# Performance work log

Measured on AMD Instinct MI355X. Metric: run time of the kernel, lower is better.

Reference implementation:

```python
import jax, jax.numpy as jnp
import numpy as np

EPS = 1e-5
B, N, E, D, ED, F = 4096, 22, 42, 128, 32, 2048

def _ln(x, g, b):
    m = jnp.mean(x, axis=-1, keepdims=True)
    v = jnp.var(x, axis=-1, keepdims=True)
    return (x - m) * jax.lax.rsqrt(v + EPS) * g + b

def setup_inputs() -> dict:
    key = jax.random.key(0)
    ks = jax.random.split(key, 24)
    def rn(k, shp, scale=0.05):
        return jax.random.normal(k, shp, dtype=jnp.float32) * scale
    return {
        "node_features": jax.random.normal(ks[0], (B, N, D), dtype=jnp.float32),
        "edge_attr": jax.random.normal(ks[1], (B, E, ED), dtype=jnp.float32),
        "aggregation_matrix": jax.random.uniform(ks[2], (N, E), dtype=jnp.float32),
        "source_indices": jax.random.randint(ks[3], (E,), 0, N, dtype=jnp.int32),
        "target_indices": jax.random.randint(ks[4], (E,), 0, N, dtype=jnp.int32),
        # edge MLP: Linear(2D+ED -> 4*ED), ReLU, Linear(4*ED -> ED)
        "ew1": rn(ks[5], (2 * D + ED, 4 * ED)), "eb1": jnp.zeros((4 * ED,), jnp.float32),
        "ew2": rn(ks[6], (4 * ED, ED)), "eb2": jnp.zeros((ED,), jnp.float32),
        # message projection ED -> D
        "pw": rn(ks[7], (ED, D)), "pb": jnp.zeros((D,), jnp.float32),
        # gated update gates: 2D -> D each
        "rw": rn(ks[8], (2 * D, D)), "rb": jnp.zeros((D,), jnp.float32),
        "uw": rn(ks[9], (2 * D, D)), "ub": jnp.zeros((D,), jnp.float32),
        "cw": rn(ks[10], (2 * D, D)), "cb": jnp.zeros((D,), jnp.float32),
        # layernorms
        "g1": jnp.ones((D,), jnp.float32), "be1": jnp.zeros((D,), jnp.float32),
        "g2": jnp.ones((D,), jnp.float32), "be2": jnp.zeros((D,), jnp.float32),
        # FFN D -> F -> D
        "fw1": rn(ks[11], (D, F)), "fb1": jnp.zeros((F,), jnp.float32),
        "fw2": rn(ks[12], (F, D)), "fb2": jnp.zeros((D,), jnp.float32),
    }

def reference(node_features, edge_attr, aggregation_matrix, source_indices, target_indices,
              ew1, eb1, ew2, eb2, pw, pb, rw, rb, uw, ub, cw, cb,
              g1, be1, g2, be2, fw1, fb1, fw2, fb2):
    normed = _ln(node_features, g1, be1)                      # [B,N,D]
    src = jnp.take(normed, source_indices, axis=1)            # [B,E,D]
    tgt = jnp.take(normed, target_indices, axis=1)            # [B,E,D]
    combined = jnp.concatenate([src, tgt, edge_attr], axis=-1)  # [B,E,2D+ED]
    h = jax.nn.relu(combined @ ew1 + eb1)
    edge_messages = h @ ew2 + eb2                             # [B,E,ED]
    aggregated = jnp.einsum('ne,bed->bnd', aggregation_matrix, edge_messages)  # [B,N,ED]
    projected = aggregated @ pw + pb                          # [B,N,D]
    # GRU-style gated update
    nm = jnp.concatenate([normed, projected], axis=-1)
    reset = jax.nn.sigmoid(nm @ rw + rb)
    update = jax.nn.sigmoid(nm @ uw + ub)
    rc = jnp.concatenate([reset * normed, projected], axis=-1)
    cand = jnp.tanh(rc @ cw + cb)
    x = node_features + (1.0 - update) * normed + update * cand
    # norm + FFN (dropout = identity in eval mode)
    n2 = _ln(x, g2, be2)
    ff = jax.nn.gelu(n2 @ fw1 + fb1, approximate=False) @ fw2 + fb2
    return (x + ff, edge_messages)
```

## Files before the change

### kernel.cpp

```cpp
#include <hip/hip_runtime.h>
#include <math.h>

#define NB 4096
#define NN 22
#define NE 42
#define DD 128
#define ED2 32
#define HH 128
#define FF 2048
#define HCHUNKS 32

typedef float f32x4 __attribute__((ext_vector_type(4)));
typedef short s16x8 __attribute__((ext_vector_type(8)));

__device__ __forceinline__ float sigmoidf_(float x){ return 1.f/(1.f+__expf(-x)); }

__device__ __forceinline__ unsigned short f2bf(float f){
  unsigned u = __float_as_uint(f);
  u += 0x7fffu + ((u >> 16) & 1u);
  return (unsigned short)(u >> 16);
}
__device__ __forceinline__ float bf2f(unsigned short h){
  return __uint_as_float(((unsigned)h) << 16);
}
__device__ __forceinline__ float gelu_f(float x){
  float x2 = x*x;
  float inner = fmaf(0.044715f*x2, x, x);
  float p = __builtin_amdgcn_exp2f(2.3022085f*inner);
  float t = __builtin_amdgcn_rcpf(p + 1.f);
  return fmaf(-x, t, x);
}

__device__ __forceinline__ void gld16(const void* g, void* l){
  __builtin_amdgcn_global_load_lds((__attribute__((address_space(1))) void*)g,
                                   (__attribute__((address_space(3))) void*)l, 16, 0, 0);
}
template<int BYTES, int NW>
__device__ __forceinline__ void stage_lds(void* lbase, const void* gbase, int wave, int lane){
  const int per = BYTES / NW;
  const int ni  = per / 1024;
  const char* g = (const char*)gbase + wave*per + lane*16;
  char* l = (char*)lbase + wave*per;
  #pragma unroll
  for (int i=0;i<ni;i++) gld16(g + i*1024, l + i*1024);
}

#define S_VMCNT(N) { asm volatile("s_waitcnt vmcnt(" #N ")" ::: "memory"); __builtin_amdgcn_sched_barrier(0); }
#define S_LGKM0()  { asm volatile("s_waitcnt lgkmcnt(0)" ::: "memory"); __builtin_amdgcn_sched_barrier(0); }
#define RAW_BAR()  { asm volatile("s_waitcnt lgkmcnt(0)" ::: "memory"); __builtin_amdgcn_sched_barrier(0); __builtin_amdgcn_s_barrier(); __builtin_amdgcn_sched_barrier(0); }

__device__ __forceinline__ int fragidx128(int c, int k){
  return ((c>>4)*4 + (k>>5))*512 + (((k>>3)&3)*16 + (c&15))*8 + (k&7);
}
__device__ __forceinline__ int fragidx64(int c, int k){
  return ((c>>4)*2 + (k>>5))*512 + (((k>>3)&3)*16 + (c&15))*8 + (k&7);
}

__global__ __launch_bounds__(256) void wconv_kernel(
    const float* __restrict__ fw1, const float* __restrict__ fw2,
    const float* __restrict__ ew1, const float* __restrict__ ew2,
    const float* __restrict__ rw, const float* __restrict__ uw, const float* __restrict__ cw,
    const float* __restrict__ pw, const float* __restrict__ aggm,
    unsigned short* __restrict__ w1t, unsigned short* __restrict__ w2b,
    unsigned short* __restrict__ ewc, unsigned short* __restrict__ ew2c,
    unsigned short* __restrict__ gw,
    unsigned short* __restrict__ tailf, unsigned short* __restrict__ pwf,
    unsigned short* __restrict__ aggmf)
{
  const int idx = blockIdx.x*256 + threadIdx.x;
  {
    const int k = idx >> 11, j = idx & 2047;
    w1t[(j>>7)*16384 + fragidx128(j&127, k)] = f2bf(fw1[idx]);
  }
  {
    const int kg = idx >> 7, c = idx & 127;
    w2b[(kg>>6)*8192 + fragidx64(c, kg&63)] = f2bf(fw2[idx]);
  }
  if (idx < 32768) {
    const int c2 = idx >> 7, k = idx & 127;
    const int part = c2 >> 7, c = c2 & 127;
    const float v = ew1[(part*128 + k)*DD + c];
    ewc[part*16384 + ((k>>5)*8 + (c>>4))*512 + (((k>>3)&3)*16 + (c&15))*8 + (k&7)] = f2bf(v);
  }
  if (idx < 4096) {
    const int m = idx & 31, k = idx >> 5;
    ew2c[fragidx128(m, k)] = f2bf(ew2[k*ED2 + m]);
  }
  if (idx < 4096) {
    const int k = idx >> 7, c = idx & 127;
    const int u = (c>>4)*512 + ((k>>3)*16 + (c&15))*8 + (k&7);
    tailf[u] = f2bf(ew1[(256 + k)*DD + c]);
    pwf[u]  = f2bf(pw[k*DD + c]);
  }
  if (idx < 2048) {
    const int n = idx >> 6, e = idx & 63;
    const float v = (n < NN && e < NE) ? aggm[n*NE + e] : 0.f;
    aggmf[(n>>4)*1024 + (e>>5)*512 + (((e>>3)&3)*16 + (n&15))*8 + (e&7)] = f2bf(v);
  }
  if (idx < 98304) {
    const int gate = idx >> 15;
    const int rem  = idx & 32767;
    const int half = rem >> 14, c = (rem >> 7) & 127, k = rem & 127;
    const float* wsrc = (gate==0) ? rw : ((gate==1) ? uw : cw);
    const float v = wsrc[(half*128 + k)*128 + c];
    gw[gate*32768 + half*16384 + (k>>6)*8192 + fragidx64(c, k&63)] = f2bf(v);
  }
}

__global__ __launch_bounds__(512) void edge_mfma_kernel(
    const float* __restrict__ nf, const float* __restrict__ ea,
    const int* __restrict__ src, const int* __restrict__ tgt,
    const float* __restrict__ eb1, const float* __restrict__ eb2,
    const float* __restrict__ pb,
    const unsigned short* __restrict__ ewc2,
    const unsigned short* __restrict__ ew2c,
    const unsigned short* __restrict__ tailf,
    const unsigned short* __restrict__ pwf,
    const unsigned short* __restrict__ aggmf,
    const float* __restrict__ g1, const float* __restrict__ be1,
    float* __restrict__ out_em, float* __restrict__ out_x)
{
  const int t = threadIdx.x, lane = t & 63, wave = t >> 6;
  const int wv = wave & 3;
  const int bb = wave >> 2;
  const int b  = blockIdx.x*2 + bb;
  const int th = t & 255;

  __shared__ __align__(16) char s_lds[76160];
  unsigned short* s_w0  = (unsigned short*)(s_lds);
  unsigned short* s_w1  = (unsigned short*)(s_lds + 16384);
  unsigned short* s_emf = (unsigned short*)(s_lds + 16384 + bb*4096);
  unsigned short* s_ew2 = (unsigned short*)(s_lds + 32768);
  unsigned short* s_agm = (unsigned short*)(s_lds + 40960);
  char*           s_a   = s_lds + 45056 + bb*8192;
  char*           s_h   = s_lds + 45056 + bb*12288;
  unsigned short* s_eaf = (unsigned short*)(s_lds + 69632 + bb*3072);
  unsigned short* s_agf = s_eaf;
  int*            s_srcA= (int*)(s_lds + 75776);
  int*            s_tgtA= (int*)(s_lds + 75968);

  stage_lds<16384,8>(s_w0, ewc2, wave, lane);
  stage_lds<8192,8>(s_ew2, ew2c, wave, lane);
  if (wave < 4) stage_lds<4096,4>(s_agm, aggmf, wave, lane);

  for (int r = wv; r < NN; r += 4) {
    const float* row = nf + ((size_t)b*NN + r)*DD;
    float x0 = row[lane], x1 = row[lane+64];
    float s = x0+x1, ss = x0*x0+x1*x1;
    #pragma unroll
    for (int off=32; off>=1; off>>=1) { s += __shfl_xor(s,off); ss += __shfl_xor(ss,off); }
    float m = s*(1.f/128.f);
    float inv = rsqrtf(ss*(1.f/128.f)-m*m + 1e-5f);
    float n0 = (x0-m)*inv*g1[lane]+be1[lane];
    float n1 = (x1-m)*inv*g1[lane+64]+be1[lane+64];
    char* base = s_a + r*256;
    const int sw = (r&7)<<4;
    *(unsigned short*)(base + ((lane*2)      ^ sw)) = f2bf(n0);
    *(unsigned short*)(base + (((lane+64)*2) ^ sw)) = f2bf(n1);
  }
  for (int i=th; i<640; i+=256) ((float*)(s_a + NN*256))[i] = 0.f;

  if (t < 48) { s_srcA[t] = (t < NE) ? src[t] : NN; s_tgtA[t] = (t < NE) ? tgt[t] : NN; }

  if (th < 168) {
    const int e = th >> 2, kb = th & 3;
    const float* p = ea + ((size_t)b*NE + e)*ED2 + kb*8;
    const float4 v0 = *(const float4*)p;
    const float4 v1 = *(const float4*)(p+4);
    unsigned long long lo = (unsigned long long)f2bf(v0.x) | ((unsigned long long)f2bf(v0.y)<<16)
                          | ((unsigned long long)f2bf(v0.z)<<32) | ((unsigned long long)f2bf(v0.w)<<48);
    unsigned long long hi = (unsigned long long)f2bf(v1.x) | ((unsigned long long)f2bf(v1.y)<<16)
                          | ((unsigned long long)f2bf(v1.z)<<32) | ((unsigned long long)f2bf(v1.w)<<48);
    unsigned long long* dst = (unsigned long long*)(s_eaf + (e>>4)*512 + (kb*16 + (e&15))*8);
    dst[0] = lo; dst[1] = hi;
  } else if (th < 192) {
    const int idx = th - 168;
    const int kb = idx / 6, er = 10 + idx % 6;
    unsigned long long* dst = (unsigned long long*)(s_eaf + 2*512 + (kb*16 + er)*8);
    dst[0] = 0ull; dst[1] = 0ull;
  }

  __syncthreads();

  const int frow = lane & 15;
  const int gsel = (lane >> 4) << 4;
  const int nt0 = wv*2;

  int rowS[3], rowT[3];
  #pragma unroll
  for (int mt=0; mt<3; ++mt){
    rowS[mt] = s_srcA[mt*16 + frow];
    rowT[mt] = s_tgtA[mt*16 + frow];
  }

  f32x4 hacc[3][2];
  #pragma unroll
  for (int mt=0; mt<3; ++mt){
    hacc[mt][0] = (f32x4){0.f,0.f,0.f,0.f};
    hacc[mt][1] = (f32x4){0.f,0.f,0.f,0.f};
  }

  #define HROUND(WCP, ROWS, KOFF) { \
    const unsigned short* wc_ = (WCP); \
    _Pragma("unroll") \
    for (int mt=0; mt<3; ++mt){ \
      const int r_ = (ROWS)[mt]; \
      const int sw_ = (r_&7)<<4; \
      const s16x8 a0 = *(const s16x8*)(s_a + r_*256 + (((KOFF) + gsel)^sw_)); \
      const s16x8 a1 = *(const s16x8*)(s_a + r_*256 + (((KOFF) + 64 + gsel)^sw_)); \
      _Pragma("unroll") \
      for (int ntl=0; ntl<2; ++ntl){ \
        const s16x8 b0 = *(const s16x8*)(wc_ + (    nt0+ntl)*512 + lane*8); \
        const s16x8 b1 = *(const s16x8*)(wc_ + (8 + nt0+ntl)*512 + lane*8); \
        hacc[mt][ntl] = __builtin_amdgcn_mfma_f32_16x16x32_bf16(a0, b0, hacc[mt][ntl], 0,0,0); \
        hacc[mt][ntl] = __builtin_amdgcn_mfma_f32_16x16x32_bf16(a1, b1, hacc[mt][ntl], 0,0,0); \
      } \
    } }

  stage_lds<16384,8>(s_w1, ewc2 + 8192, wave, lane);
  HROUND(s_w0, rowS, 0);
  S_VMCNT(0);
  RAW_BAR();
  stage_lds<16384,8>(s_w0, ewc2 + 16384, wave, lane);
  HROUND(s_w1, rowS, 128);
  S_VMCNT(0);
  RAW_BAR();
  stage_lds<16384,8>(s_w1, ewc2 + 24576, wave, lane);
  HROUND(s_w0, rowT, 0);
  S_VMCNT(0);
  RAW_BAR();
  stage_lds<8192,8>(s_w0, tailf, wave, lane);
  HROUND(s_w1, rowT, 128);
  S_VMCNT(0);
  RAW_BAR();
  #undef HROUND

  { uint4 z; z.x=0u; z.y=0u; z.z=0u; z.w=0u; *(uint4*)(s_lds + 16384 + t*16) = z; }
  #pragma unroll
  for (int mt=0; mt<3; ++mt){
    const s16x8 ae = *(const s16x8*)(s_eaf + mt*512 + lane*8);
    #pragma unroll
    for (int ntl=0; ntl<2; ++ntl){
      const s16x8 bt = *(const s16x8*)(s_w0 + (nt0+ntl)*512 + lane*8);
      hacc[mt][ntl] = __builtin_amdgcn_mfma_f32_16x16x32_bf16(ae, bt, hacc[mt][ntl], 0,0,0);
    }
  }
  #pragma unroll
  for (int mt=0; mt<3; ++mt){
    #pragma unroll
    for (int ntl=0; ntl<2; ++ntl){
      const int c = (nt0+ntl)*16 + frow;
      const float e1 = eb1[c];
      #pragma unroll
      for (int reg=0; reg<4; ++reg){
        const int e = mt*16 + (lane>>4)*4 + reg;
        const float v = fmaxf(hacc[mt][ntl][reg] + e1, 0.f);
        *(unsigned short*)(s_h + e*256 + ((c*2) ^ ((e&7)<<4))) = (e < NE) ? f2bf(v) : (unsigned short)0;
      }
    }
  }
  RAW_BAR();

  stage_lds<8192,8>(s_w0, pwf, wave, lane);
  for (int id = wv; id < 6; id += 4) {
    const int mt = id >> 1, ntn = id & 1;
    f32x4 acc2 = (f32x4){0.f,0.f,0.f,0.f};
    #pragma unroll
    for (int ks=0; ks<4; ++ks){
      const s16x8 av = *(const s16x8*)(s_h + (mt*16 + frow)*256 + ((ks*64 + gsel) ^ ((frow&7)<<4)));
      const s16x8 bv = *(const s16x8*)(s_ew2 + (ntn*4+ks)*512 + lane*8);
      acc2 = __builtin_amdgcn_mfma_f32_16x16x32_bf16(av, bv, acc2, 0,0,0);
    }
    const int mc = ntn*16 + frow;
    const float bias = eb2[mc];
    #pragma unroll
    for (int reg=0; reg<4; ++reg){
      const int e = mt*16 + (lane>>4)*4 + reg;
      if (e < NE) {
        const float v = acc2[reg] + bias;
        out_em[((size_t)b*NE + e)*ED2 + mc] = v;
        s_emf[(mc>>4)*1024 + (e>>5)*512 + (((e>>3)&3)*16 + (mc&15))*8 + (e&7)] = f2bf(v);
      }
    }
  }
  S_VMCNT(0);
  RAW_BAR();

  {
    const int mt = wv >> 1, ntn = wv & 1;
    f32x4 acc3 = (f32x4){0.f,0.f,0.f,0.f};
    #pragma unroll
    for (int ks=0; ks<2; ++ks){
      const s16x8 av = *(const s16x8*)(s_agm + (mt*2+ks)*512 + lane*8);
      const s16x8 bv = *(const s16x8*)(s_emf + (ntn*2+ks)*512 + lane*8);
      acc3 = __builtin_amdgcn_mfma_f32_16x16x32_bf16(av, bv, acc3, 0,0,0);
    }
    const int mc = ntn*16 + frow;
    #pragma unroll
    for (int reg=0; reg<4; ++reg){
      const int n = mt*16 + (lane>>4)*4 + reg;
      s_agf[(n>>4)*512 + (((mc>>3)&3)*16 + (n&15))*8 + (mc&7)] = f2bf(acc3[reg]);
    }
  }
  RAW_BAR();

  const unsigned short* s_pw = (const unsigned short*)s_lds;
  #pragma unroll
  for (int ii=0; ii<4; ++ii){
    const int id = wv + ii*4;
    const int mt = id >> 3, nt = id & 7;
    const s16x8 av = *(const s16x8*)(s_agf + mt*512 + lane*8);
    const s16x8 bv = *(const s16x8*)(s_pw + nt*512 + lane*8);
    f32x4 a4 = __builtin_amdgcn_mfma_f32_16x16x32_bf16(av, bv, (f32x4){0.f,0.f,0.f,0.f}, 0,0,0);
    const int c = nt*16 + frow;
    const float pbv = pb[c];
    #pragma unroll
    for (int reg=0; reg<4; ++reg){
      const int n = mt*16 + (lane>>4)*4 + reg;
      *(unsigned short*)(s_h + n*256 + ((c*2) ^ ((n&7)<<4))) = f2bf(a4[reg] + pbv);
    }
  }
  RAW_BAR();

  for (int o=th; o<NN*16; o+=256){
    const int n = o>>4, cell = o&15;
    const int k0 = (cell>>2)*32 + (cell&3)*8;
    const uint4 v = *(const uint4*)(s_h + n*256 + ((k0*2) ^ ((n&7)<<4)));
    *(uint4*)((char*)out_x + (((size_t)b*NN + n)*512) + cell*16) = v;
  }
}

__global__ __launch_bounds__(256) void gate_mfma_kernel(
    const float* __restrict__ nf,
    const float* __restrict__ rb, const float* __restrict__ ub, const float* __restrict__ cbv,
    const float* __restrict__ g1, const float* __restrict__ be1,
    const unsigned short* __restrict__ gw,
    float* __restrict__ out_x)
{
  const int t=threadIdx.x, lane=t&63, wave=t>>6;
  const size_t row0 = (size_t)blockIdx.x * 64;
  const int wrow = wave*16;

  __shared__ __align__(16) unsigned short s_nb[8192];
  __shared__ __align__(16) unsigned short s_w[2][8192];
  __shared__ float s_mean[64], s_inv[64];
  unsigned short* s_pb = s_w[1];

  const char* gwb = (const char*)gw;

  stage_lds<16384,4>(s_w[0], gwb, wave, lane);

  for (int i=t; i<1024; i+=256){
    const int r = i>>4, cell = i&15;
    ((uint4*)s_pb)[((r>>4)*4 + (cell>>2))*64 + (cell&3)*16 + (r&15)] =
      *((const uint4*)(out_x + (row0+r)*DD) + cell);
  }

  for (int r16=0; r16<16; ++r16){
    const int row = wrow + r16;
    const float* xr = nf + (row0+row)*DD;
    float x0=xr[lane], x1=xr[lane+64];
    float s=x0+x1, ss=x0*x0+x1*x1;
    #pragma unroll
    for (int off=32; off>=1; off>>=1){ s+=__shfl_xor(s,off); ss+=__shfl_xor(ss,off); }
    float m=s*(1.f/128.f);
    float inv=rsqrtf(ss*(1.f/128.f)-m*m+1e-5f);
    if (lane==0){ s_mean[row]=m; s_inv[row]=inv; }
    float n0=(x0-m)*inv*g1[lane]+be1[lane];
    float n1=(x1-m)*inv*g1[lane+64]+be1[lane+64];
    const int mt = row>>4, fr = row&15;
    const int ks = lane>>5, g = (lane>>3)&3, j = lane&7;
    s_nb[(mt*4+ks)*512   + (g*16+fr)*8 + j] = f2bf(n0);
    s_nb[(mt*4+ks+2)*512 + (g*16+fr)*8 + j] = f2bf(n1);
  }
  __syncthreads();

  s16x8 aN[4], aP[4];
  #pragma unroll
  for (int kk=0; kk<4; ++kk){
    aN[kk] = *(const s16x8*)(s_nb + (wave*4+kk)*512 + lane*8);
    aP[kk] = *(const s16x8*)(s_pb + (wave*4+kk)*512 + lane*8);
  }
  RAW_BAR();

  f32x4 accR[8], accU[8], accC[8];
  #pragma unroll
  for (int nt=0; nt<8; ++nt){
    const int col = nt*16 + (lane&15);
    accR[nt] = (f32x4){rb[col],rb[col],rb[col],rb[col]};
    accU[nt] = (f32x4){ub[col],ub[col],ub[col],ub[col]};
    accC[nt] = (f32x4){cbv[col],cbv[col],cbv[col],cbv[col]};
  }

  #define GSTAGE(S, NEXT, ACC, A0, A1) { \
    if (NEXT) stage_lds<16384,4>(s_w[((S)+1)&1], gwb + ((S)+1)*16384, wave, lane); \
    unsigned short* sb = s_w[(S)&1]; \
    _Pragma("unroll") for (int nt=0;nt<8;++nt){ \
      const s16x8 b0 = *(const s16x8*)(sb + (nt*2+0)*512 + lane*8); \
      ACC[nt] = __builtin_amdgcn_mfma_f32_16x16x32_bf16(A0, b0, ACC[nt], 0,0,0); \
      const s16x8 b1 = *(const s16x8*)(sb + (nt*2+1)*512 + lane*8); \
      ACC[nt] = __builtin_amdgcn_mfma_f32_16x16x32_bf16(A1, b1, ACC[nt], 0,0,0); } \
    S_VMCNT(0); \
    RAW_BAR(); }

  GSTAGE(0, 1, accR, aN[0], aN[1]);
  GSTAGE(1, 1, accR, aN[2], aN[3]);
  GSTAGE(2, 1, accR, aP[0], aP[1]);
  GSTAGE(3, 1, accR, aP[2], aP[3]);

  #pragma unroll
  for (int nt=0; nt<8; ++nt){
    #pragma unroll
    for (int reg=0; reg<4; ++reg){
      const float r_ = sigmoidf_(accR[nt][reg]);
      const int frA = (lane>>4)*4 + reg;
      const int ks = nt>>1, g = ((nt&1)<<1) | ((lane&15)>>3), j = lane&7;
      unsigned short* p = s_nb + (wave*4+ks)*512 + (g*16+frA)*8 + j;
      *p = f2bf(r_ * bf2f(*p));
    }
  }
  s16x8 aRC[4];
  #pragma unroll
  for (int kk=0; kk<4; ++kk)
    aRC[kk] = *(const s16x8*)(s_nb + (wave*4+kk)*512 + lane*8);

  GSTAGE(4, 1, accU, aN[0], aN[1]);
  GSTAGE(5, 1, accU, aN[2], aN[3]);
  GSTAGE(6, 1, accU, aP[0], aP[1]);
  GSTAGE(7, 1, accU, aP[2], aP[3]);
  GSTAGE(8, 1, accC, aRC[0], aRC[1]);
  GSTAGE(9, 1, accC, aRC[2], aRC[3]);
  GSTAGE(10, 1, accC, aP[0], aP[1]);
  GSTAGE(11, 0, accC, aP[2], aP[3]);
  #undef GSTAGE

  #pragma unroll
  for (int nt=0; nt<8; ++nt){
    const int col = nt*16 + (lane&15);
    const float gg = g1[col], bb = be1[col];
    #pragma unroll
    for (int reg=0; reg<4; ++reg){
      const int rowl = wrow + (lane>>4)*4 + reg;
      const size_t grow = row0 + rowl;
      const float u_ = sigmoidf_(accU[nt][reg]);
      const float cand = tanhf(accC[nt][reg]);
      const float nfv = nf[grow*DD + col];
      const float nv = (nfv - s_mean[rowl])*s_inv[rowl]*gg + bb;
      out_x[grow*DD + col] = nfv + (1.f-u_)*nv + u_*cand;
    }
  }
}

__global__ __launch_bounds__(512) void ffn_mfma_kernel(
    float* __restrict__ out_x,
    const float* __restrict__ g2, const float* __restrict__ be2,
    const float* __restrict__ fb1, const float* __restrict__ fb2,
    const unsigned short* __restrict__ w1t,
    const unsigned short* __restrict__ w2b)
{
  const int t = threadIdx.x, lane = t & 63, wave = t >> 6;
  const size_t row0 = (size_t)blockIdx.x * 128;
  const int wrow = wave * 16;
  const int rg = wave >> 1, cg = wave & 1;

  __shared__ __align__(16) unsigned short s_buf[2][16384];
  __shared__ __align__(16) unsigned short s_hid[8192];

  stage_lds<16384,8>(s_buf[0],        w1t, wave, lane);
  stage_lds<16384,8>(s_buf[0] + 8192, w2b, wave, lane);

  for (int r16 = 0; r16 < 16; ++r16) {
    const int row = wrow + r16;
    const float* xr = out_x + (row0+row)*DD;
    float x0 = xr[lane], x1 = xr[lane+64];
    float s = x0+x1, ss = x0*x0+x1*x1;
    #pragma unroll
    for (int off=32; off>=1; off>>=1){ s+=__shfl_xor(s,off); ss+=__shfl_xor(ss,off); }
    float m = s*(1.f/128.f);
    float inv = rsqrtf(ss*(1.f/128.f)-m*m+1e-5f);
    float n0 = (x0-m)*inv*g2[lane]+be2[lane];
    float n1 = (x1-m)*inv*g2[lane+64]+be2[lane+64];
    const int fr = row&15;
    const int ks = lane>>5, g = (lane>>3)&3, j = lane&7;
    unsigned short* dst = s_buf[1] + (wave>>2)*8192;
    const int wv = wave & 3;
    dst[(wv*4+ks)*512   + (g*16+fr)*8 + j] = f2bf(n0);
    dst[(wv*4+ks+2)*512 + (g*16+fr)*8 + j] = f2bf(n1);
  }
  __syncthreads();

  const int frow = lane & 15;
  const int q = lane >> 4;

  s16x8 aN[2][4];
  #pragma unroll
  for (int mt=0; mt<2; ++mt){
    const int m = rg*2 + mt;
    const unsigned short* srcb = s_buf[1] + (m>>2)*8192;
    #pragma unroll
    for (int ks=0; ks<4; ++ks)
      aN[mt][ks] = *(const s16x8*)(srcb + ((m&3)*4+ks)*512 + lane*8);
  }
  RAW_BAR();

  const int hb = (rg*4 + cg)*512 + (((q>>1)*16 + frow)*8) + (q&1)*4;

  f32x4 accO[2][4];
  #pragma unroll
  for (int mt=0; mt<2; ++mt)
    #pragma unroll
    for (int nt=0; nt<4; ++nt)
      accO[mt][nt] = (f32x4){0.f,0.f,0.f,0.f};

  for (int hc = 0; hc < HCHUNKS; ++hc) {
    const unsigned short* cur = s_buf[hc & 1];
    unsigned short* nxt = s_buf[(hc + 1) & 1];
    if (hc < HCHUNKS-1) {
      stage_lds<16384,8>(nxt,        w1t + (hc+1)*8192, wave, lane);
      stage_lds<16384,8>(nxt + 8192, w2b + (hc+1)*8192, wave, lane);
    }

    f32x4 acc1[2][2];
    #pragma unroll
    for (int nt=0; nt<2; ++nt){
      const float4 bv = *(const float4*)(fb1 + hc*64 + cg*32 + nt*16 + (q<<2));
      acc1[0][nt] = (f32x4){bv.x, bv.y, bv.z, bv.w};
      acc1[1][nt] = acc1[0][nt];
    }
    #pragma unroll
    for (int nt=0; nt<2; ++nt){
      #pragma unroll
      for (int ks=0; ks<4; ++ks){
        const s16x8 ww = *(const s16x8*)(cur + ((cg*2+nt)*4+ks)*512 + lane*8);
        acc1[0][nt] = __builtin_amdgcn_mfma_f32_16x16x32_bf16(ww, aN[0][ks], acc1[0][nt], 0,0,0);
        acc1[1][nt] = __builtin_amdgcn_mfma_f32_16x16x32_bf16(ww, aN[1][ks], acc1[1][nt], 0,0,0);
      }
    }
    #pragma unroll
    for (int mt=0; mt<2; ++mt){
      #pragma unroll
      for (int nt=0; nt<2; ++nt){
        const float e0 = gelu_f(acc1[mt][nt][0]);
        const float e1 = gelu_f(acc1[mt][nt][1]);
        const float e2 = gelu_f(acc1[mt][nt][2]);
        const float e3 = gelu_f(acc1[mt][nt][3]);
        unsigned plo, phi;
        asm("v_cvt_pk_bf16_f32 %0, %1, %2" : "=v"(plo) : "v"(e0), "v"(e1));
        asm("v_cvt_pk_bf16_f32 %0, %1, %2" : "=v"(phi) : "v"(e2), "v"(e3));
        uint2 pk; pk.x = plo; pk.y = phi;
        *(uint2*)((char*)s_hid + (hb + mt*1024 + nt*256)*2) = pk;
      }
    }
    RAW_BAR();

    s16x8 aH[2][2];
    #pragma unroll
    for (int mt=0; mt<2; ++mt)
      #pragma unroll
      for (int ks=0; ks<2; ++ks)
        aH[mt][ks] = *(const s16x8*)(s_hid + ((rg*2+mt)*2+ks)*512 + lane*8);
    #pragma unroll
    for (int nt=0; nt<4; ++nt){
      #pragma unroll
      for (int ks=0; ks<2; ++ks){
        const s16x8 bb = *(const s16x8*)(cur + 8192 + ((cg*4+nt)*2+ks)*512 + lane*8);
        accO[0][nt] = __builtin_amdgcn_mfma_f32_16x16x32_bf16(aH[0][ks], bb, accO[0][nt], 0,0,0);
        accO[1][nt] = __builtin_amdgcn_mfma_f32_16x16x32_bf16(aH[1][ks], bb, accO[1][nt], 0,0,0);
      }
    }
    S_VMCNT(0);
    RAW_BAR();
  }

  #pragma unroll
  for (int mt=0; mt<2; ++mt){
    #pragma unroll
    for (int nt=0; nt<4; ++nt){
      const int colg = cg*64 + nt*16 + frow;
      const float bias = fb2[colg];
      #pragma unroll
      for (int reg=0; reg<4; ++reg){
        const size_t row = row0 + rg*32 + mt*16 + q*4 + reg;
        const float xo = out_x[row*DD + colg];
        out_x[row*DD + colg] = xo + bias + accO[mt][nt][reg];
      }
    }
  }
}

extern "C" void kernel_launch(void* const* d_in, const int* in_sizes, int n_in,
                              void* d_out, int out_size, void* d_ws, size_t ws_size,
                              hipStream_t stream) {
  const float* nf  = (const float*)d_in[0];
  const float* ea  = (const float*)d_in[1];
  const float* agg = (const float*)d_in[2];
  const int*   src = (const int*)d_in[3];
  const int*   tgt = (const int*)d_in[4];
  const float* ew1 = (const float*)d_in[5];
  const float* eb1 = (const float*)d_in[6];
  const float* ew2 = (const float*)d_in[7];
  const float* eb2 = (const float*)d_in[8];
  const float* pw  = (const float*)d_in[9];
  const float* pb  = (const float*)d_in[10];
  const float* rw  = (const float*)d_in[11];
  const float* rb  = (const float*)d_in[12];
  const float* uw  = (const float*)d_in[13];
  const float* ub  = (const float*)d_in[14];
  const float* cw  = (const float*)d_in[15];
  const float* cbv = (const float*)d_in[16];
  const float* g1  = (const float*)d_in[17];
  const float* be1 = (const float*)d_in[18];
  const float* g2  = (const float*)d_in[19];
  const float* be2 = (const float*)d_in[20];
  const float* fw1 = (const float*)d_in[21];
  const float* fb1 = (const float*)d_in[22];
  const float* fw2 = (const float*)d_in[23];
  const float* fb2 = (const float*)d_in[24];

  float* out_x  = (float*)d_out;
  float* out_em = (float*)d_out + (size_t)NB*NN*DD;

  unsigned short* w1t  = (unsigned short*)d_ws;
  unsigned short* w2b  = w1t + (size_t)FF*DD;
  unsigned short* ewc  = w2b + (size_t)FF*DD;
  unsigned short* ew2c = ewc + (size_t)256*128;
  unsigned short* gw   = ew2c + (size_t)32*128;
  unsigned short* tailf= gw + (size_t)3*32768;
  unsigned short* pwf  = tailf + 4096;
  unsigned short* aggmf= pwf + 4096;

  hipLaunchKernelGGL(wconv_kernel, dim3(1024), dim3(256), 0, stream,
                     fw1, fw2, ew1, ew2, rw, uw, cw, pw, agg,
                     w1t, w2b, ewc, ew2c, gw, tailf, pwf, aggmf);
  hipLaunchKernelGGL(edge_mfma_kernel, dim3(NB/2), dim3(512), 0, stream,
                     nf, ea, src, tgt, eb1, eb2, pb, ewc, ew2c, tailf, pwf, aggmf,
                     g1, be1, out_em, out_x);
  hipLaunchKernelGGL(gate_mfma_kernel, dim3(NB*NN/64), dim3(256), 0, stream,
                     nf, rb, ub, cbv, g1, be1, gw, out_x);
  hipLaunchKernelGGL(ffn_mfma_kernel, dim3(NB*NN/128), dim3(512), 0, stream,
                     out_x, g2, be2, fb1, fb2, w1t, w2b);
}
```

Baseline: 300.4 us.

## Keep FFN hidden activations in registers by permuting W1 columns, drop LDS round-trip

Permutes the fw1 column order during weight conversion so that the MFMA output fragment of the first FFN GEMM already matches the A-operand layout needed by the second GEMM. The GELU results are packed straight into registers instead of going through the s_hid LDS buffer and its barrier on every hidden chunk. Each wave now computes a split-K partial over all 128 output columns, which doubles the output accumulators and adds a cross-wave reduction through LDS at the end. This trades extra registers and a final reduction for removing one LDS write, read and barrier per chunk.

Measured after the change: 369.8 us. 1.23x slower.

```diff
diff --git a/kernel.cpp b/kernel.cpp
--- a/kernel.cpp
+++ b/kernel.cpp
@@ -69,8 +69,10 @@
 {
   const int idx = blockIdx.x*256 + threadIdx.x;
   {
-    const int k = idx >> 11, j = idx & 2047;
-    w1t[(j>>7)*16384 + fragidx128(j&127, k)] = f2bf(fw1[idx]);
+    const int k = idx >> 11, jd = idx & 2047;
+    const int cl = jd & 63;
+    const int jsrc = (jd & ~63) | (cl & 32) | (((cl>>2)&3)<<3) | (((cl>>4)&1)<<2) | (cl&3);
+    w1t[(jd>>7)*16384 + fragidx128(jd&127, k)] = f2bf(fw1[k*2048 + jsrc]);
   }
   {
     const int kg = idx >> 7, c = idx & 127;
@@ -464,7 +466,6 @@
   const int rg = wave >> 1, cg = wave & 1;
 
   __shared__ __align__(16) unsigned short s_buf[2][16384];
-  __shared__ __align__(16) unsigned short s_hid[8192];
 
   stage_lds<16384,8>(s_buf[0],        w1t, wave, lane);
   stage_lds<16384,8>(s_buf[0] + 8192, w2b, wave, lane);
@@ -503,13 +504,11 @@
   }
   RAW_BAR();
 
-  const int hb = (rg*4 + cg)*512 + (((q>>1)*16 + frow)*8) + (q&1)*4;
-
-  f32x4 accO[2][4];
+  f32x4 accO[2][8];
   #pragma unroll
   for (int mt=0; mt<2; ++mt)
     #pragma unroll
-    for (int nt=0; nt<4; ++nt)
+    for (int nt=0; nt<8; ++nt)
       accO[mt][nt] = (f32x4){0.f,0.f,0.f,0.f};
 
   for (int hc = 0; hc < HCHUNKS; ++hc) {
@@ -523,7 +522,7 @@
     f32x4 acc1[2][2];
     #pragma unroll
     for (int nt=0; nt<2; ++nt){
-      const float4 bv = *(const float4*)(fb1 + hc*64 + cg*32 + nt*16 + (q<<2));
+      const float4 bv = *(const float4*)(fb1 + hc*64 + cg*32 + (q<<3) + (nt<<2));
       acc1[0][nt] = (f32x4){bv.x, bv.y, bv.z, bv.w};
       acc1[1][nt] = acc1[0][nt];
     }
@@ -538,51 +537,70 @@
     }
     #pragma unroll
     for (int mt=0; mt<2; ++mt){
-      #pragma unroll
-      for (int nt=0; nt<2; ++nt){
-        const float e0 = gelu_f(acc1[mt][nt][0]);
-        const float e1 = gelu_f(acc1[mt][nt][1]);
-        const float e2 = gelu_f(acc1[mt][nt][2]);
-        const float e3 = gelu_f(acc1[mt][nt][3]);
+      uint4 hv;
+      {
+        const float e0 = gelu_f(acc1[mt][0][0]);
+        const float e1 = gelu_f(acc1[mt][0][1]);
+        const float e2 = gelu_f(acc1[mt][0][2]);
+        const float e3 = gelu_f(acc1[mt][0][3]);
         unsigned plo, phi;
         asm("v_cvt_pk_bf16_f32 %0, %1, %2" : "=v"(plo) : "v"(e0), "v"(e1));
         asm("v_cvt_pk_bf16_f32 %0, %1, %2" : "=v"(phi) : "v"(e2), "v"(e3));
-        uint2 pk; pk.x = plo; pk.y = phi;
-        *(uint2*)((char*)s_hid + (hb + mt*1024 + nt*256)*2) = pk;
-      }
-    }
-    RAW_BAR();
-
-    s16x8 aH[2][2];
-    #pragma unroll
-    for (int mt=0; mt<2; ++mt)
+        hv.x = plo; hv.y = phi;
+      }
+      {
+        const float e0 = gelu_f(acc1[mt][1][0]);
+        const float e1 = gelu_f(acc1[mt][1][1]);
+        const float e2 = gelu_f(acc1[mt][1][2]);
+        const float e3 = gelu_f(acc1[mt][1][3]);
+        unsigned plo, phi;
+        asm("v_cvt_pk_bf16_f32 %0, %1, %2" : "=v"(plo) : "v"(e0), "v"(e1));
+        asm("v_cvt_pk_bf16_f32 %0, %1, %2" : "=v"(phi) : "v"(e2), "v"(e3));
+        hv.z = plo; hv.w = phi;
+      }
+      s16x8 aH;
+      __builtin_memcpy(&aH, &hv, 16);
       #pragma unroll
-      for (int ks=0; ks<2; ++ks)
-        aH[mt][ks] = *(const s16x8*)(s_hid + ((rg*2+mt)*2+ks)*512 + lane*8);
-    #pragma unroll
-    for (int nt=0; nt<4; ++nt){
-      #pragma unroll
-      for (int ks=0; ks<2; ++ks){
-        const s16x8 bb = *(const s16x8*)(cur + 8192 + ((cg*4+nt)*2+ks)*512 + lane*8);
-        accO[0][nt] = __builtin_amdgcn_mfma_f32_16x16x32_bf16(aH[0][ks], bb, accO[0][nt], 0,0,0);
-        accO[1][nt] = __builtin_amdgcn_mfma_f32_16x16x32_bf16(aH[1][ks], bb, accO[1][nt], 0,0,0);
+      for (int nt=0; nt<8; ++nt){
+        const s16x8 bb = *(const s16x8*)(cur + 8192 + (nt*2+cg)*512 + lane*8);
+        accO[mt][nt] = __builtin_amdgcn_mfma_f32_16x16x32_bf16(aH, bb, accO[mt][nt], 0,0,0);
       }
     }
     S_VMCNT(0);
     RAW_BAR();
   }
 
-  #pragma unroll
-  for (int mt=0; mt<2; ++mt){
-    #pragma unroll
-    for (int nt=0; nt<4; ++nt){
-      const int colg = cg*64 + nt*16 + frow;
-      const float bias = fb2[colg];
+  float* s_red = (float*)s_buf;
+  {
+    float* wr = s_red + rg*4096 + cg*2048;
+    #pragma unroll
+    for (int mt=0; mt<2; ++mt){
       #pragma unroll
-      for (int reg=0; reg<4; ++reg){
-        const size_t row = row0 + rg*32 + mt*16 + q*4 + reg;
-        const float xo = out_x[row*DD + colg];
-        out_x[row*DD + colg] = xo + bias + accO[mt][nt][reg];
+      for (int nl=0; nl<4; ++nl){
+        const int nt = (cg==0) ? (4+nl) : nl;
+        #pragma unroll
+        for (int reg=0; reg<4; ++reg)
+          wr[((mt*4+nl)*4+reg)*64 + lane] = accO[mt][nt][reg];
+      }
+    }
+  }
+  RAW_BAR();
+  {
+    const float* rd = s_red + rg*4096 + (1-cg)*2048;
+    #pragma unroll
+    for (int mt=0; mt<2; ++mt){
+      #pragma unroll
+      for (int nl=0; nl<4; ++nl){
+        const int nt = cg*4 + nl;
+        const int colg = nt*16 + frow;
+        const float bias = fb2[colg];
+        #pragma unroll
+        for (int reg=0; reg<4; ++reg){
+          const size_t row = row0 + rg*32 + mt*16 + q*4 + reg;
+          const float xo = out_x[row*DD + colg];
+          out_x[row*DD + colg] = xo + bias + accO[mt][nt][reg]
+                                 + rd[((mt*4+nl)*4+reg)*64 + lane];
+        }
       }
     }
   }
```
